# Kernel optimization log

Hardware: AMD Instinct MI355X
Metric: run time of the kernel (lower is better)

The kernel has to match this reference:

```python
import jax, jax.numpy as jnp
import numpy as np

K = 2  # kernel_size == stride, padding=0, dilation=1 -> non-overlapping 2x2x2 blocks


def setup_inputs() -> dict:
    key = jax.random.key(0)
    # (b, c, s, w, h) volumetric batch
    x = jax.random.normal(key, (8, 1, 64, 192, 192), dtype=jnp.float32)
    return {"x": x}


def _extract_blocks(x, k):
    # Faithful to extract_patches_3d with stride==kernel, padding=0, dilation=1:
    # the double unfold + permute + flat view yields rows ordered (b, c, do, ho, wo),
    # each row the flattened k*k*k patch.
    b, c, s, w, h = x.shape
    blk = x.reshape(b, c, s // k, k, w // k, k, h // k, k)
    blk = blk.transpose(0, 1, 2, 4, 6, 3, 5, 7)  # (b,c,do,ho,wo,k,k,k)
    return blk.reshape(-1, k * k * k)  # (N, k^3)


def reference(x):
    b, c, s, w, h = x.shape
    data = _extract_blocks(x, K)            # (N, 8)
    mean = jnp.mean(data, axis=0)           # (8,)
    centered = data - mean
    # torch.svd: data = U S V^T ; jax returns vh = V^T
    _, _, vh = jnp.linalg.svd(centered, full_matrices=False)
    pca_components = vh[:1].T               # (8, n_components=1)
    reduced = centered @ pca_components     # (N, 1)
    out = reduced.reshape(b, c, s // K, w // K, h // K)
    return out, mean, pca_components
```

## Files before the change

### kernel.cpp

```cpp
#include <hip/hip_runtime.h>

constexpr int NB     = 8 * 32 * 96 * 96;
constexpr int NPAIR  = NB / 2;
constexpr int NACC   = 44;
constexpr int GRID_A = 1024;
constexpr int TPB    = 256;
constexpr int GRID_C = 1024;

__global__ __launch_bounds__(TPB)
void reduce_kernel(const float* __restrict__ x, float* __restrict__ partials) {
  float acc[NACC];
#pragma unroll
  for (int i = 0; i < NACC; ++i) acc[i] = 0.0f;

  int tid = blockIdx.x * TPB + threadIdx.x;
  const int stride = GRID_A * TPB;
  for (int p = tid; p < NPAIR; p += stride) {
    int hp = p % 48;
    int t1 = p / 48;
    int wo = t1 % 96;
    int t2 = t1 / 96;
    int so = t2 % 32;
    int b  = t2 / 32;
    const float* base = x + (((b * 64 + 2 * so) * 192 + 2 * wo) * 192 + 4 * hp);
    float4 r0 = *(const float4*)(base);
    float4 r1 = *(const float4*)(base + 192);
    float4 r2 = *(const float4*)(base + 192 * 192);
    float4 r3 = *(const float4*)(base + 192 * 192 + 192);
    float v0[8] = {r0.x, r0.y, r1.x, r1.y, r2.x, r2.y, r3.x, r3.y};
    float v1[8] = {r0.z, r0.w, r1.z, r1.w, r2.z, r2.w, r3.z, r3.w};
#pragma unroll
    for (int a = 0; a < 8; ++a) acc[a] += v0[a] + v1[a];
    int k = 8;
#pragma unroll
    for (int a = 0; a < 8; ++a)
#pragma unroll
      for (int q = a; q < 8; ++q) acc[k++] += v0[a] * v0[q] + v1[a] * v1[q];
  }

#pragma unroll
  for (int i = 0; i < NACC; ++i) {
    float v = acc[i];
    for (int off = 32; off >= 1; off >>= 1) v += __shfl_down(v, off, 64);
    acc[i] = v;
  }
  __shared__ float lds[4][NACC];
  int lane = threadIdx.x & 63;
  int wv   = threadIdx.x >> 6;
  if (lane == 0) {
#pragma unroll
    for (int i = 0; i < NACC; ++i) lds[wv][i] = acc[i];
  }
  __syncthreads();
  if (threadIdx.x < NACC) {
    float s = lds[0][threadIdx.x] + lds[1][threadIdx.x] +
              lds[2][threadIdx.x] + lds[3][threadIdx.x];
    partials[threadIdx.x * GRID_A + blockIdx.x] = s;
  }
}

__global__ __launch_bounds__(TPB)
void mid_reduce_kernel(const float* __restrict__ partials, double* __restrict__ sums_d) {
  int a = blockIdx.x;
  int t = threadIdx.x;
  const float* row = partials + a * GRID_A;
  double s = (double)row[t] + (double)row[t + 256] +
             (double)row[t + 512] + (double)row[t + 768];
  for (int off = 32; off >= 1; off >>= 1) s += __shfl_down(s, off, 64);
  __shared__ double lds[4];
  if ((t & 63) == 0) lds[t >> 6] = s;
  __syncthreads();
  if (t == 0) sums_d[a] = lds[0] + lds[1] + lds[2] + lds[3];
}

__device__ __forceinline__ float rdlane(float x, int lane) {
  return __int_as_float(__builtin_amdgcn_readlane(__float_as_int(x), lane));
}

template <int P, int Q>
__device__ __forceinline__ void jrot(const float (&r)[8], float& ct, float& st) {
  float app = rdlane(r[P], P);
  float aqq = rdlane(r[Q], Q);
  float apq = rdlane(r[Q], P);
  float theta = (aqq - app) * 0.5f * __builtin_amdgcn_rcpf(apq);
  float root  = __builtin_amdgcn_sqrtf(theta * theta + 1.0f);
  float tmag  = __builtin_amdgcn_rcpf(fabsf(theta) + root);
  float tt    = copysignf(tmag, theta);
  float c     = __builtin_amdgcn_rsqf(tt * tt + 1.0f);
  float s     = tt * c;
  bool zero   = (apq == 0.0f);
  ct = zero ? 1.0f : c;
  st = zero ? 0.0f : s;
}

template <int P, int Q>
__device__ __forceinline__ void jcol(float (&r)[8], float (&v)[8], float c, float s) {
  float rp = r[P], rq = r[Q];
  r[P] = c * rp - s * rq;
  r[Q] = s * rp + c * rq;
  float vp = v[P], vq = v[Q];
  v[P] = c * vp - s * vq;
  v[Q] = s * vp + c * vq;
}

template <int P0,int Q0,int P1,int Q1,int P2,int Q2,int P3,int Q3>
__device__ __forceinline__ void jacobi_round(float (&r)[8], float (&v)[8], int i) {
  float c0,s0,c1,s1,c2,s2,c3,s3;
  jrot<P0,Q0>(r, c0, s0);
  jrot<P1,Q1>(r, c1, s1);
  jrot<P2,Q2>(r, c2, s2);
  jrot<P3,Q3>(r, c3, s3);
  jcol<P0,Q0>(r, v, c0, s0);
  jcol<P1,Q1>(r, v, c1, s1);
  jcol<P2,Q2>(r, v, c2, s2);
  jcol<P3,Q3>(r, v, c3, s3);
  float alpha = 1.0f, beta = 0.0f;
  int plane = i;
  if (i == P0) { alpha = c0; beta = -s0; plane = Q0; }
  if (i == Q0) { alpha = c0; beta =  s0; plane = P0; }
  if (i == P1) { alpha = c1; beta = -s1; plane = Q1; }
  if (i == Q1) { alpha = c1; beta =  s1; plane = P1; }
  if (i == P2) { alpha = c2; beta = -s2; plane = Q2; }
  if (i == Q2) { alpha = c2; beta =  s2; plane = P2; }
  if (i == P3) { alpha = c3; beta = -s3; plane = Q3; }
  if (i == Q3) { alpha = c3; beta =  s3; plane = P3; }
  float prow[8];
#pragma unroll
  for (int j = 0; j < 8; ++j) prow[j] = __shfl(r[j], plane, 64);
#pragma unroll
  for (int j = 0; j < 8; ++j) r[j] = alpha * r[j] + beta * prow[j];
}

__global__ __launch_bounds__(TPB)
void project_solve_kernel(const float* __restrict__ x,
                          const double* __restrict__ sums_d,
                          float* __restrict__ out,
                          float* __restrict__ out_tail) {
  __shared__ double sums[NACC];
  __shared__ float s_res[9];
  int tid = threadIdx.x;

  if (tid < NACC) sums[tid] = sums_d[tid];
  __syncthreads();

  if (tid < 64) {
    const int i = tid & 7;
    const double invN = 1.0 / (double)NB;
    double mean[8];
#pragma unroll
    for (int j = 0; j < 8; ++j) mean[j] = sums[j] * invN;

    double mean_i = mean[0];
#pragma unroll
    for (int k = 1; k < 8; ++k) if (i == k) mean_i = mean[k];

    double rowd[8];
#pragma unroll
    for (int j = 0; j < 8; ++j) {
      int p = i < j ? i : j;
      int q = i < j ? j : i;
      int idx = 8 + p * 8 - (p * (p - 1)) / 2 + (q - p);
      rowd[j] = sums[idx] - (double)NB * mean_i * mean[j];
    }
    double tr = 0.0;
#pragma unroll
    for (int k = 0; k < 8; ++k) tr += __shfl(rowd[k], k, 64);
    double shift = tr * 0.125;

    float r[8], v[8];
#pragma unroll
    for (int j = 0; j < 8; ++j) {
      double d = rowd[j] - (j == i ? shift : 0.0);
      r[j] = (float)(d * (1.0 / 1536.0));
      v[j] = (j == i) ? 1.0f : 0.0f;
    }

#pragma unroll 1
    for (int sweep = 0; sweep < 6; ++sweep) {
      jacobi_round<7,0, 1,6, 2,5, 3,4>(r, v, i);
      jacobi_round<7,1, 2,0, 3,6, 4,5>(r, v, i);
      jacobi_round<7,2, 3,1, 4,0, 5,6>(r, v, i);
      jacobi_round<7,3, 4,2, 5,1, 6,0>(r, v, i);
      jacobi_round<7,4, 5,3, 6,2, 0,1>(r, v, i);
      jacobi_round<7,5, 6,4, 0,3, 1,2>(r, v, i);
      jacobi_round<7,6, 0,5, 1,4, 2,3>(r, v, i);
    }

    float diag[8];
#pragma unroll
    for (int k = 0; k < 8; ++k) diag[k] = rdlane(r[k], k);
    int best = 0; float bd = diag[0];
#pragma unroll
    for (int k = 1; k < 8; ++k) if (diag[k] > bd) { bd = diag[k]; best = k; }
    float vi = v[0];
#pragma unroll
    for (int k = 1; k < 8; ++k) if (best == k) vi = v[k];
    float vec[8];
#pragma unroll
    for (int k = 0; k < 8; ++k) vec[k] = rdlane(vi, k);
    float nrm2 = 0.0f;
#pragma unroll
    for (int k = 0; k < 8; ++k) nrm2 += vec[k] * vec[k];
    float inv = 1.0f / sqrtf(nrm2);
#pragma unroll
    for (int k = 0; k < 8; ++k) vec[k] *= inv;
    int m = 0; float am = fabsf(vec[0]);
#pragma unroll
    for (int k = 1; k < 8; ++k) { float a = fabsf(vec[k]); if (a > am) { am = a; m = k; } }
    float vm = vec[0];
#pragma unroll
    for (int k = 1; k < 8; ++k) if (m == k) vm = vec[k];
    if (vm > 0.0f) {
#pragma unroll
      for (int k = 0; k < 8; ++k) vec[k] = -vec[k];
    }
    double c0d = 0.0;
#pragma unroll
    for (int k = 0; k < 8; ++k) c0d += mean[k] * (double)vec[k];

    float mi = (float)mean[0];
#pragma unroll
    for (int k = 1; k < 8; ++k) if (i == k) mi = (float)mean[k];
    float vl = vec[0];
#pragma unroll
    for (int k = 1; k < 8; ++k) if (i == k) vl = vec[k];

    if (tid < 8) {
      s_res[tid] = vl;
      if (blockIdx.x == 0) {
        out_tail[tid]     = mi;
        out_tail[8 + tid] = vl;
      }
    }
    if (tid == 0) s_res[8] = (float)c0d;
  }
  __syncthreads();

  float w0 = s_res[0], w1 = s_res[1], w2 = s_res[2], w3 = s_res[3];
  float w4 = s_res[4], w5 = s_res[5], w6 = s_res[6], w7 = s_res[7];
  float c0 = s_res[8];
  float2* out2 = (float2*)out;
  const int stride = GRID_C * TPB;
  for (int p = blockIdx.x * TPB + tid; p < NPAIR; p += stride) {
    int hp = p % 48;
    int t1 = p / 48;
    int wo = t1 % 96;
    int t2 = t1 / 96;
    int so = t2 % 32;
    int b  = t2 / 32;
    const float* base = x + (((b * 64 + 2 * so) * 192 + 2 * wo) * 192 + 4 * hp);
    float4 r0 = *(const float4*)(base);
    float4 r1 = *(const float4*)(base + 192);
    float4 r2 = *(const float4*)(base + 192 * 192);
    float4 r3 = *(const float4*)(base + 192 * 192 + 192);
    float o0 = r0.x * w0 + r0.y * w1 + r1.x * w2 + r1.y * w3
             + r2.x * w4 + r2.y * w5 + r3.x * w6 + r3.y * w7 - c0;
    float o1 = r0.z * w0 + r0.w * w1 + r1.z * w2 + r1.w * w3
             + r2.z * w4 + r2.w * w5 + r3.z * w6 + r3.w * w7 - c0;
    out2[p] = make_float2(o0, o1);
  }
}

extern "C" void kernel_launch(void* const* d_in, const int* in_sizes, int n_in,
                              void* d_out, int out_size, void* d_ws, size_t ws_size,
                              hipStream_t stream) {
  (void)in_sizes; (void)n_in; (void)out_size; (void)ws_size;
  const float* x = (const float*)d_in[0];
  float* out = (float*)d_out;
  float* partials = (float*)d_ws;
  double* sums_d  = (double*)(partials + NACC * GRID_A);

  reduce_kernel<<<GRID_A, TPB, 0, stream>>>(x, partials);
  mid_reduce_kernel<<<NACC, TPB, 0, stream>>>(partials, sums_d);
  project_solve_kernel<<<GRID_C, TPB, 0, stream>>>(x, sums_d, out, out + NB);
}
```

Measured before the change: 57.60 us.

## Move eigen-solve into last-block of mid reduce, slim projection kernel

The Jacobi eigen-solve no longer runs redundantly in every block of the projection kernel. It now runs once, in the last block of the mid-reduce kernel, chosen with an atomic counter and thread fences, and writes the weights to a small workspace buffer. The projection kernel just loads 9 floats and streams the data, with its grid doubled and launch bounds raised to improve occupancy. The cost is a workspace counter reset inside the first kernel, plus a serial tail on one block of the middle kernel.

```diff
diff --git a/kernel.cpp b/kernel.cpp
--- a/kernel.cpp
+++ b/kernel.cpp
@@ -5,10 +5,13 @@
 constexpr int NACC   = 44;
 constexpr int GRID_A = 1024;
 constexpr int TPB    = 256;
-constexpr int GRID_C = 1024;
-
-__global__ __launch_bounds__(TPB)
-void reduce_kernel(const float* __restrict__ x, float* __restrict__ partials) {
+constexpr int GRID_P = 2048;
+
+__global__ __launch_bounds__(TPB, 4)
+void reduce_kernel(const float* __restrict__ x, float* __restrict__ partials,
+                   unsigned int* __restrict__ ctr) {
+  if (blockIdx.x == 0 && threadIdx.x == 0) *ctr = 0u;
+
   float acc[NACC];
 #pragma unroll
   for (int i = 0; i < NACC; ++i) acc[i] = 0.0f;
@@ -57,20 +60,6 @@
               lds[2][threadIdx.x] + lds[3][threadIdx.x];
     partials[threadIdx.x * GRID_A + blockIdx.x] = s;
   }
-}
-
-__global__ __launch_bounds__(TPB)
-void mid_reduce_kernel(const float* __restrict__ partials, double* __restrict__ sums_d) {
-  int a = blockIdx.x;
-  int t = threadIdx.x;
-  const float* row = partials + a * GRID_A;
-  double s = (double)row[t] + (double)row[t + 256] +
-             (double)row[t + 512] + (double)row[t + 768];
-  for (int off = 32; off >= 1; off >>= 1) s += __shfl_down(s, off, 64);
-  __shared__ double lds[4];
-  if ((t & 63) == 0) lds[t >> 6] = s;
-  __syncthreads();
-  if (t == 0) sums_d[a] = lds[0] + lds[1] + lds[2] + lds[3];
 }
 
 __device__ __forceinline__ float rdlane(float x, int lane) {
@@ -132,116 +121,135 @@
 }
 
 __global__ __launch_bounds__(TPB)
-void project_solve_kernel(const float* __restrict__ x,
-                          const double* __restrict__ sums_d,
-                          float* __restrict__ out,
-                          float* __restrict__ out_tail) {
+void mid_solve_kernel(const float* __restrict__ partials, double* __restrict__ sums_d,
+                      unsigned int* __restrict__ ctr, float* __restrict__ res,
+                      float* __restrict__ out_tail) {
+  int a = blockIdx.x;
+  int t = threadIdx.x;
+  const float* row = partials + a * GRID_A;
+  double s = (double)row[t] + (double)row[t + 256] +
+             (double)row[t + 512] + (double)row[t + 768];
+  for (int off = 32; off >= 1; off >>= 1) s += __shfl_down(s, off, 64);
+  __shared__ double lds[4];
+  __shared__ bool is_last;
+  if ((t & 63) == 0) lds[t >> 6] = s;
+  __syncthreads();
+  if (t == 0) {
+    sums_d[a] = lds[0] + lds[1] + lds[2] + lds[3];
+    __threadfence();
+    unsigned int old = atomicAdd(ctr, 1u);
+    is_last = (old == (unsigned int)(NACC - 1));
+  }
+  __syncthreads();
+  if (!is_last) return;
+  __threadfence();
+
   __shared__ double sums[NACC];
+  if (t < NACC) sums[t] = sums_d[t];
+  __syncthreads();
+  if (t >= 64) return;
+
+  const int i = t & 7;
+  const double invN = 1.0 / (double)NB;
+  double mean[8];
+#pragma unroll
+  for (int j = 0; j < 8; ++j) mean[j] = sums[j] * invN;
+
+  double mean_i = mean[0];
+#pragma unroll
+  for (int k = 1; k < 8; ++k) if (i == k) mean_i = mean[k];
+
+  double rowd[8];
+#pragma unroll
+  for (int j = 0; j < 8; ++j) {
+    int p = i < j ? i : j;
+    int q = i < j ? j : i;
+    int idx = 8 + p * 8 - (p * (p - 1)) / 2 + (q - p);
+    rowd[j] = sums[idx] - (double)NB * mean_i * mean[j];
+  }
+  double tr = 0.0;
+#pragma unroll
+  for (int k = 0; k < 8; ++k) tr += __shfl(rowd[k], k, 64);
+  double shift = tr * 0.125;
+
+  float r[8], v[8];
+#pragma unroll
+  for (int j = 0; j < 8; ++j) {
+    double d = rowd[j] - (j == i ? shift : 0.0);
+    r[j] = (float)(d * (1.0 / 1536.0));
+    v[j] = (j == i) ? 1.0f : 0.0f;
+  }
+
+#pragma unroll 1
+  for (int sweep = 0; sweep < 6; ++sweep) {
+    jacobi_round<7,0, 1,6, 2,5, 3,4>(r, v, i);
+    jacobi_round<7,1, 2,0, 3,6, 4,5>(r, v, i);
+    jacobi_round<7,2, 3,1, 4,0, 5,6>(r, v, i);
+    jacobi_round<7,3, 4,2, 5,1, 6,0>(r, v, i);
+    jacobi_round<7,4, 5,3, 6,2, 0,1>(r, v, i);
+    jacobi_round<7,5, 6,4, 0,3, 1,2>(r, v, i);
+    jacobi_round<7,6, 0,5, 1,4, 2,3>(r, v, i);
+  }
+
+  float diag[8];
+#pragma unroll
+  for (int k = 0; k < 8; ++k) diag[k] = rdlane(r[k], k);
+  int best = 0; float bd = diag[0];
+#pragma unroll
+  for (int k = 1; k < 8; ++k) if (diag[k] > bd) { bd = diag[k]; best = k; }
+  float vi = v[0];
+#pragma unroll
+  for (int k = 1; k < 8; ++k) if (best == k) vi = v[k];
+  float vec[8];
+#pragma unroll
+  for (int k = 0; k < 8; ++k) vec[k] = rdlane(vi, k);
+  float nrm2 = 0.0f;
+#pragma unroll
+  for (int k = 0; k < 8; ++k) nrm2 += vec[k] * vec[k];
+  float inv = 1.0f / sqrtf(nrm2);
+#pragma unroll
+  for (int k = 0; k < 8; ++k) vec[k] *= inv;
+  int m = 0; float am = fabsf(vec[0]);
+#pragma unroll
+  for (int k = 1; k < 8; ++k) { float aa = fabsf(vec[k]); if (aa > am) { am = aa; m = k; } }
+  float vm = vec[0];
+#pragma unroll
+  for (int k = 1; k < 8; ++k) if (m == k) vm = vec[k];
+  if (vm > 0.0f) {
+#pragma unroll
+    for (int k = 0; k < 8; ++k) vec[k] = -vec[k];
+  }
+  double c0d = 0.0;
+#pragma unroll
+  for (int k = 0; k < 8; ++k) c0d += mean[k] * (double)vec[k];
+
+  float mi = (float)mean[0];
+#pragma unroll
+  for (int k = 1; k < 8; ++k) if (i == k) mi = (float)mean[k];
+  float vl = vec[0];
+#pragma unroll
+  for (int k = 1; k < 8; ++k) if (i == k) vl = vec[k];
+
+  if (t < 8) {
+    res[t]            = vl;
+    out_tail[t]       = mi;
+    out_tail[8 + t]   = vl;
+  }
+  if (t == 0) res[8] = (float)c0d;
+}
+
+__global__ __launch_bounds__(TPB, 8)
+void project_kernel(const float* __restrict__ x, const float* __restrict__ res,
+                    float* __restrict__ out) {
   __shared__ float s_res[9];
-  int tid = threadIdx.x;
-
-  if (tid < NACC) sums[tid] = sums_d[tid];
-  __syncthreads();
-
-  if (tid < 64) {
-    const int i = tid & 7;
-    const double invN = 1.0 / (double)NB;
-    double mean[8];
-#pragma unroll
-    for (int j = 0; j < 8; ++j) mean[j] = sums[j] * invN;
-
-    double mean_i = mean[0];
-#pragma unroll
-    for (int k = 1; k < 8; ++k) if (i == k) mean_i = mean[k];
-
-    double rowd[8];
-#pragma unroll
-    for (int j = 0; j < 8; ++j) {
-      int p = i < j ? i : j;
-      int q = i < j ? j : i;
-      int idx = 8 + p * 8 - (p * (p - 1)) / 2 + (q - p);
-      rowd[j] = sums[idx] - (double)NB * mean_i * mean[j];
-    }
-    double tr = 0.0;
-#pragma unroll
-    for (int k = 0; k < 8; ++k) tr += __shfl(rowd[k], k, 64);
-    double shift = tr * 0.125;
-
-    float r[8], v[8];
-#pragma unroll
-    for (int j = 0; j < 8; ++j) {
-      double d = rowd[j] - (j == i ? shift : 0.0);
-      r[j] = (float)(d * (1.0 / 1536.0));
-      v[j] = (j == i) ? 1.0f : 0.0f;
-    }
-
-#pragma unroll 1
-    for (int sweep = 0; sweep < 6; ++sweep) {
-      jacobi_round<7,0, 1,6, 2,5, 3,4>(r, v, i);
-      jacobi_round<7,1, 2,0, 3,6, 4,5>(r, v, i);
-      jacobi_round<7,2, 3,1, 4,0, 5,6>(r, v, i);
-      jacobi_round<7,3, 4,2, 5,1, 6,0>(r, v, i);
-      jacobi_round<7,4, 5,3, 6,2, 0,1>(r, v, i);
-      jacobi_round<7,5, 6,4, 0,3, 1,2>(r, v, i);
-      jacobi_round<7,6, 0,5, 1,4, 2,3>(r, v, i);
-    }
-
-    float diag[8];
-#pragma unroll
-    for (int k = 0; k < 8; ++k) diag[k] = rdlane(r[k], k);
-    int best = 0; float bd = diag[0];
-#pragma unroll
-    for (int k = 1; k < 8; ++k) if (diag[k] > bd) { bd = diag[k]; best = k; }
-    float vi = v[0];
-#pragma unroll
-    for (int k = 1; k < 8; ++k) if (best == k) vi = v[k];
-    float vec[8];
-#pragma unroll
-    for (int k = 0; k < 8; ++k) vec[k] = rdlane(vi, k);
-    float nrm2 = 0.0f;
-#pragma unroll
-    for (int k = 0; k < 8; ++k) nrm2 += vec[k] * vec[k];
-    float inv = 1.0f / sqrtf(nrm2);
-#pragma unroll
-    for (int k = 0; k < 8; ++k) vec[k] *= inv;
-    int m = 0; float am = fabsf(vec[0]);
-#pragma unroll
-    for (int k = 1; k < 8; ++k) { float a = fabsf(vec[k]); if (a > am) { am = a; m = k; } }
-    float vm = vec[0];
-#pragma unroll
-    for (int k = 1; k < 8; ++k) if (m == k) vm = vec[k];
-    if (vm > 0.0f) {
-#pragma unroll
-      for (int k = 0; k < 8; ++k) vec[k] = -vec[k];
-    }
-    double c0d = 0.0;
-#pragma unroll
-    for (int k = 0; k < 8; ++k) c0d += mean[k] * (double)vec[k];
-
-    float mi = (float)mean[0];
-#pragma unroll
-    for (int k = 1; k < 8; ++k) if (i == k) mi = (float)mean[k];
-    float vl = vec[0];
-#pragma unroll
-    for (int k = 1; k < 8; ++k) if (i == k) vl = vec[k];
-
-    if (tid < 8) {
-      s_res[tid] = vl;
-      if (blockIdx.x == 0) {
-        out_tail[tid]     = mi;
-        out_tail[8 + tid] = vl;
-      }
-    }
-    if (tid == 0) s_res[8] = (float)c0d;
-  }
-  __syncthreads();
-
+  if (threadIdx.x < 9) s_res[threadIdx.x] = res[threadIdx.x];
+  __syncthreads();
   float w0 = s_res[0], w1 = s_res[1], w2 = s_res[2], w3 = s_res[3];
   float w4 = s_res[4], w5 = s_res[5], w6 = s_res[6], w7 = s_res[7];
   float c0 = s_res[8];
   float2* out2 = (float2*)out;
-  const int stride = GRID_C * TPB;
-  for (int p = blockIdx.x * TPB + tid; p < NPAIR; p += stride) {
+  const int stride = GRID_P * TPB;
+  for (int p = blockIdx.x * TPB + threadIdx.x; p < NPAIR; p += stride) {
     int hp = p % 48;
     int t1 = p / 48;
     int wo = t1 % 96;
@@ -267,10 +275,12 @@
   (void)in_sizes; (void)n_in; (void)out_size; (void)ws_size;
   const float* x = (const float*)d_in[0];
   float* out = (float*)d_out;
-  float* partials = (float*)d_ws;
-  double* sums_d  = (double*)(partials + NACC * GRID_A);
-
-  reduce_kernel<<<GRID_A, TPB, 0, stream>>>(x, partials);
-  mid_reduce_kernel<<<NACC, TPB, 0, stream>>>(partials, sums_d);
-  project_solve_kernel<<<GRID_C, TPB, 0, stream>>>(x, sums_d, out, out + NB);
-}
+  float* partials      = (float*)d_ws;
+  double* sums_d       = (double*)(partials + NACC * GRID_A);
+  float* res           = (float*)(sums_d + NACC);
+  unsigned int* ctr    = (unsigned int*)(res + 16);
+
+  reduce_kernel<<<GRID_A, TPB, 0, stream>>>(x, partials, ctr);
+  mid_solve_kernel<<<NACC, TPB, 0, stream>>>(partials, sums_d, ctr, res, out + NB);
+  project_kernel<<<GRID_P, TPB, 0, stream>>>(x, res, out);
+}
```

Measured after the change: 63.59 us. 1.1x slower.
